# Kernel optimization log

Measured on AMD Instinct MI355X. Metric: run time of the kernel, lower is better.

The kernel has to match this reference:

```python
import jax, jax.numpy as jnp
import numpy as np

N_NODES = 50000
N_EDGES = 800000
EMB = 384            # EMBEDDING_DIM
NODE_F = EMB + 4     # 388
EDGE_F = EMB + 1     # 385
HEADS = 2
HID = 32             # per-head out_channels
HC = HEADS * HID     # 64
EDGE_IN = 2 * HC + EMB  # 512 classifier input
NEG_SLOPE = 0.2


def setup_inputs() -> dict:
    key = jax.random.key(0)
    ks = jax.random.split(key, 16)
    s = 0.05
    return {
        "x": jax.random.normal(ks[0], (N_NODES, NODE_F), dtype=jnp.float32),
        "edge_index": jax.random.randint(ks[1], (2, N_EDGES), 0, N_NODES, dtype=jnp.int32),
        "edge_attr": jax.random.uniform(ks[2], (N_EDGES, EDGE_F), dtype=jnp.float32),
        # GATv2Conv params
        "lin_l_w": jax.random.normal(ks[3], (NODE_F, HC), dtype=jnp.float32) * s,
        "lin_l_b": jnp.zeros((HC,), jnp.float32),
        "lin_r_w": jax.random.normal(ks[4], (NODE_F, HC), dtype=jnp.float32) * s,
        "lin_r_b": jnp.zeros((HC,), jnp.float32),
        "lin_e_w": jax.random.normal(ks[5], (EDGE_F, HC), dtype=jnp.float32) * s,
        "att": jax.random.normal(ks[6], (HEADS, HID), dtype=jnp.float32) * s,
        "conv_b": jnp.zeros((HC,), jnp.float32),
        # edge classifier MLP
        "mlp1_w": jax.random.normal(ks[7], (EDGE_IN, 64), dtype=jnp.float32) * s,
        "mlp1_b": jnp.zeros((64,), jnp.float32),
        "mlp2_w": jax.random.normal(ks[8], (64, 3), dtype=jnp.float32) * s,
        "mlp2_b": jnp.zeros((3,), jnp.float32),
    }


def _gatv2(x, edge_index, edge_attr, lin_l_w, lin_l_b, lin_r_w, lin_r_b,
           lin_e_w, att, conv_b):
    N = x.shape[0]
    src, tgt = edge_index[0], edge_index[1]
    # PyG add_self_loops with fill_value='mean': self-loop edge_attr is the
    # mean of incoming edge attributes per target node (0 if none).
    ones = jnp.ones((edge_attr.shape[0],), edge_attr.dtype)
    cnt = jax.ops.segment_sum(ones, tgt, num_segments=N)
    loop_attr = jax.ops.segment_sum(edge_attr, tgt, num_segments=N)
    loop_attr = loop_attr / jnp.maximum(cnt, 1.0)[:, None]
    ar = jnp.arange(N, dtype=src.dtype)
    src = jnp.concatenate([src, ar])
    tgt = jnp.concatenate([tgt, ar])
    ea = jnp.concatenate([edge_attr, loop_attr], axis=0)  # [E+N, EDGE_F]

    xl = (x @ lin_l_w + lin_l_b).reshape(N, HEADS, HID)  # source transform
    xr = (x @ lin_r_w + lin_r_b).reshape(N, HEADS, HID)  # target transform
    ee = (ea @ lin_e_w).reshape(-1, HEADS, HID)

    # GATv2 scoring: att . leaky_relu(x_j + x_i + e_ij)
    m = jax.nn.leaky_relu(xl[src] + xr[tgt] + ee, NEG_SLOPE)  # [E', H, C]
    score = jnp.einsum('ehc,hc->eh', m, att)                  # [E', H]
    # segment softmax over incoming edges of each target node
    smax = jax.ops.segment_max(score, tgt, num_segments=N)
    ex = jnp.exp(score - smax[tgt])
    ssum = jax.ops.segment_sum(ex, tgt, num_segments=N)
    alpha = ex / (ssum[tgt] + 1e-16)                          # [E', H]
    out = jax.ops.segment_sum(alpha[:, :, None] * xl[src], tgt, num_segments=N)
    return out.reshape(N, HC) + conv_b


def reference(x, edge_index, edge_attr, lin_l_w, lin_l_b, lin_r_w, lin_r_b,
              lin_e_w, att, conv_b, mlp1_w, mlp1_b, mlp2_w, mlp2_b):
    h = jax.nn.relu(_gatv2(x, edge_index, edge_attr, lin_l_w, lin_l_b,
                           lin_r_w, lin_r_b, lin_e_w, att, conv_b))
    # prediction edges == graph edges; query emb = edge_attr[:, :-1]
    src_e = h[edge_index[0]]
    tgt_e = h[edge_index[1]]
    q = edge_attr[:, :-1]
    e = jnp.concatenate([src_e, tgt_e, q], axis=1)  # [E, 512]
    e = jax.nn.relu(e @ mlp1_w + mlp1_b)
    logits = e @ mlp2_w + mlp2_b                    # [E, 3]
    probs = jax.nn.softmax(logits, axis=1)
    trust = 0.0 * probs[:, 0] + 0.5 * probs[:, 1] + 1.0 * probs[:, 2]
    return trust
```

## Files before the change

### kernel.cpp

```cpp
#include <hip/hip_runtime.h>

#define N_NODES 50000
#define N_EDGES 800000
#define NODE_F  388
#define EDGE_F  385
#define HC      64
#define KRED    384
#define NKT     6
#define NB      196

#define O_XLB     0L
#define O_XRB     1600000L
#define O_HAB     3200000L
#define O_HBB     4800000L
#define O_EXE     6400000L
#define O_EESUM   8000000L
#define O_SSUM    11200000L
#define O_DEG     11300000L
#define O_CURSOR  11350000L
#define O_ROWPTR  11410000L
#define O_BSUM    11470000L
#define O_CSRE    11480000L
#define O_CSRS    12280000L
#define O_CSRT    13080000L
#define O_WT      13900000L
#define O_WT2     13930000L
#define O_QW      13960000L

typedef __attribute__((ext_vector_type(8))) short bf8;
typedef __attribute__((ext_vector_type(4))) float f4;

typedef __attribute__((address_space(1))) const unsigned char ga_u8;
typedef __attribute__((address_space(3))) unsigned char lds_u8;

static __device__ __forceinline__ void gload_lds16(const void* g, void* l) {
    __builtin_amdgcn_global_load_lds((ga_u8*)g, (lds_u8*)l, 16, 0, 0);
}

static __device__ __forceinline__ unsigned short f2bf(float f) {
    unsigned u = __float_as_uint(f);
    u += 0x7FFFu + ((u >> 16) & 1u);
    return (unsigned short)(u >> 16);
}
static __device__ __forceinline__ float bf2f(unsigned short h) {
    return __uint_as_float(((unsigned)h) << 16);
}
static __device__ __forceinline__ unsigned cvtpk(float lo, float hi) {
    unsigned r;
    asm("v_cvt_pk_bf16_f32 %0, %1, %2" : "=v"(r) : "v"(lo), "v"(hi));
    return r;
}
static __device__ __forceinline__ void raw_barrier() {
    __builtin_amdgcn_sched_barrier(0);
    __builtin_amdgcn_s_barrier();
    __builtin_amdgcn_sched_barrier(0);
}

__global__ __launch_bounds__(256) void k_prep(
    const float* __restrict__ we, const float* __restrict__ w1,
    const float* __restrict__ wl, const float* __restrict__ wr,
    unsigned short* __restrict__ wt, unsigned short* __restrict__ wt2)
{
    int half = blockIdx.x / 96;
    int gid = (blockIdx.x - half * 96) * 256 + threadIdx.x;
    int c  = gid / 192;
    int k  = 2 * (gid - c * 192);
    float f0, f1;
    if (half == 0) {
        if (c < HC) {
            f0 = we[(long)k * HC + c];
            f1 = we[(long)(k + 1) * HC + c];
        } else {
            f0 = w1[(long)(128 + k) * HC + (c - HC)];
            f1 = w1[(long)(128 + k + 1) * HC + (c - HC)];
        }
        *(unsigned*)(wt + (long)c * KRED + k) =
            (unsigned)f2bf(f0) | ((unsigned)f2bf(f1) << 16);
    } else {
        const float* w = (c < HC) ? wl : wr;
        int cc = (c < HC) ? c : c - HC;
        f0 = w[(long)k * HC + cc];
        f1 = w[(long)(k + 1) * HC + cc];
        *(unsigned*)(wt2 + (long)c * KRED + k) =
            (unsigned)f2bf(f0) | ((unsigned)f2bf(f1) << 16);
    }
}

__global__ __launch_bounds__(256, 5) void k_node_lin(
    const float* __restrict__ x, const unsigned short* __restrict__ wt2,
    const float* __restrict__ wl, const float* __restrict__ wr,
    const float* __restrict__ bl, const float* __restrict__ br,
    unsigned short* __restrict__ xlb, unsigned short* __restrict__ xrb)
{
    __shared__ __align__(16) char W_s[2][16384];
    const int t = threadIdx.x;
    const int l = t & 63;
    const int w = t >> 6;
    const int n0 = blockIdx.x * 64;
    const int rb = (w & 1) * 32;
    const int cb = (w >> 1) * 64;
    const int lr = l & 15;
    const int lk = l >> 4;

    int wsrc[4];
#pragma unroll
    for (int i = 0; i < 4; ++i) {
        int c = w * 32 + i * 8 + (l >> 3);
        wsrc[i] = c * (KRED * 2) + ((((l & 7) * 16)) ^ ((l >> 3) << 4));
    }
    const char* wtb = (const char*)wt2;

    long rowx[2];
#pragma unroll
    for (int rg = 0; rg < 2; ++rg) {
        int n = n0 + rb + rg * 16 + lr;
        if (n >= N_NODES) n = N_NODES - 1;
        rowx[rg] = (long)n * NODE_F;
    }

    float af[2][16];
    bf8 fa[2][2];
    f4 acc[2][4];
#pragma unroll
    for (int rg = 0; rg < 2; ++rg)
#pragma unroll
        for (int cg = 0; cg < 4; ++cg) acc[rg][cg] = (f4)(0.f);

#define STAGE_W(kt, buf)                                                         \
    {                                                                            \
        _Pragma("unroll")                                                        \
        for (int i = 0; i < 4; ++i)                                              \
            gload_lds16(wtb + wsrc[i] + (kt) * 128, &W_s[buf][w * 4096 + i * 1024]); \
    }
#define ISSUE_AX(kt)                                                             \
    {                                                                            \
        _Pragma("unroll")                                                        \
        for (int rg = 0; rg < 2; ++rg) {                                         \
            const float* rp = x + rowx[rg] + (kt) * 64 + lk * 8;                 \
            float4 a0 = *(const float4*)(rp);                                    \
            float4 a1 = *(const float4*)(rp + 4);                                \
            float4 a2 = *(const float4*)(rp + 32);                               \
            float4 a3 = *(const float4*)(rp + 36);                               \
            af[rg][0]=a0.x; af[rg][1]=a0.y; af[rg][2]=a0.z; af[rg][3]=a0.w;      \
            af[rg][4]=a1.x; af[rg][5]=a1.y; af[rg][6]=a1.z; af[rg][7]=a1.w;      \
            af[rg][8]=a2.x; af[rg][9]=a2.y; af[rg][10]=a2.z; af[rg][11]=a2.w;    \
            af[rg][12]=a3.x; af[rg][13]=a3.y; af[rg][14]=a3.z; af[rg][15]=a3.w;  \
        }                                                                        \
    }
#define CVT_A()                                                                  \
    {                                                                            \
        _Pragma("unroll")                                                        \
        for (int rg = 0; rg < 2; ++rg)                                           \
            _Pragma("unroll")                                                    \
            for (int ks = 0; ks < 2; ++ks) {                                     \
                union { bf8 v; unsigned u[4]; } tu;                              \
                _Pragma("unroll")                                                \
                for (int p = 0; p < 4; ++p)                                      \
                    tu.u[p] = cvtpk(af[rg][ks * 8 + 2 * p], af[rg][ks * 8 + 2 * p + 1]); \
                fa[rg][ks] = tu.v;                                               \
            }                                                                    \
    }

    STAGE_W(0, 0);
    ISSUE_AX(0);

    for (int kt = 0; kt < NKT; ++kt) {
        const int buf = kt & 1;
        CVT_A();
        if (kt < NKT - 1) { STAGE_W(kt + 1, buf ^ 1); ISSUE_AX(kt + 1); }
        raw_barrier();
        __builtin_amdgcn_s_setprio(1);
#pragma unroll
        for (int ks = 0; ks < 2; ++ks) {
            const int kb = ks * 64 + lk * 16;
#pragma unroll
            for (int cg = 0; cg < 4; ++cg) {
                const int c = cb + cg * 16 + lr;
                bf8 b = *(bf8*)(&W_s[buf][c * 128 + (kb ^ ((c & 7) << 4))]);
                acc[0][cg] = __builtin_amdgcn_mfma_f32_16x16x32_bf16(fa[0][ks], b, acc[0][cg], 0, 0, 0);
                acc[1][cg] = __builtin_amdgcn_mfma_f32_16x16x32_bf16(fa[1][ks], b, acc[1][cg], 0, 0, 0);
            }
        }
        __builtin_amdgcn_s_setprio(0);
        raw_barrier();
    }

    const float* wsf = (cb == 0) ? wl : wr;
    const float* bsf = (cb == 0) ? bl : br;
    unsigned short* dst = (cb == 0) ? xlb : xrb;
    float wtail[4][4], bias[4];
#pragma unroll
    for (int cg = 0; cg < 4; ++cg) {
        int c = cg * 16 + lr;
        bias[cg] = bsf[c];
#pragma unroll
        for (int j = 0; j < 4; ++j)
            wtail[j][cg] = wsf[(long)(KRED + j) * HC + c];
    }
#pragma unroll
    for (int rg = 0; rg < 2; ++rg)
#pragma unroll
    for (int r = 0; r < 4; ++r) {
        const int n = n0 + rb + rg * 16 + lk * 4 + r;
        const int nc = (n < N_NODES) ? n : N_NODES - 1;
        float4 xt = *(const float4*)(x + (long)nc * NODE_F + KRED);
#pragma unroll
        for (int cg = 0; cg < 4; ++cg) {
            float v = acc[rg][cg][r] + bias[cg]
                    + xt.x * wtail[0][cg] + xt.y * wtail[1][cg]
                    + xt.z * wtail[2][cg] + xt.w * wtail[3][cg];
            float nb = __shfl_xor(v, 1);
            if (!(lr & 1) && n < N_NODES)
                *(unsigned*)&dst[(long)n * HC + cg * 16 + lr] = cvtpk(v, nb);
        }
    }
#undef STAGE_W
#undef ISSUE_AX
#undef CVT_A
}

__global__ __launch_bounds__(256) void k_hist(const int* __restrict__ ei, int* __restrict__ deg)
{
    int e = blockIdx.x * 256 + threadIdx.x;
    if (e < N_EDGES) atomicAdd(&deg[ei[N_EDGES + e]], 1);
}

__global__ __launch_bounds__(256) void k_scan_bsum(const int* __restrict__ deg, int* __restrict__ bsum)
{
    __shared__ int red[4];
    int i = blockIdx.x * 256 + threadIdx.x;
    int v = (i < N_NODES) ? deg[i] : 0;
    for (int m = 1; m < 64; m <<= 1) v += __shfl_xor(v, m);
    if ((threadIdx.x & 63) == 0) red[threadIdx.x >> 6] = v;
    __syncthreads();
    if (threadIdx.x == 0) bsum[blockIdx.x] = red[0] + red[1] + red[2] + red[3];
}

__global__ __launch_bounds__(256) void k_scan_boff(int* bsum)
{
    __shared__ int sc[256];
    int t = threadIdx.x;
    int v = (t < NB) ? bsum[t] : 0;
    sc[t] = v; __syncthreads();
    for (int off = 1; off < 256; off <<= 1) {
        int tv = (t >= off) ? sc[t - off] : 0;
        __syncthreads();
        sc[t] += tv;
        __syncthreads();
    }
    if (t < NB) bsum[t] = sc[t] - v;
}

__global__ __launch_bounds__(256) void k_scan_row(const int* __restrict__ deg,
                                                  const int* __restrict__ bsum,
                                                  int* __restrict__ rowptr)
{
    __shared__ int sc[256];
    int t = threadIdx.x;
    int i = blockIdx.x * 256 + t;
    int v = (i < N_NODES) ? deg[i] : 0;
    sc[t] = v; __syncthreads();
    for (int off = 1; off < 256; off <<= 1) {
        int tv = (t >= off) ? sc[t - off] : 0;
        __syncthreads();
        sc[t] += tv;
        __syncthreads();
    }
    if (i < N_NODES) rowptr[i] = bsum[blockIdx.x] + sc[t] - v;
    if (i == N_NODES - 1) rowptr[N_NODES] = N_EDGES;
}

__global__ __launch_bounds__(256) void k_scatter(const int* __restrict__ ei,
                                                 const int* __restrict__ rowptr,
                                                 int* __restrict__ cursor,
                                                 int* __restrict__ csr_e, int* __restrict__ csr_s,
                                                 int* __restrict__ csr_t)
{
    int e = blockIdx.x * 256 + threadIdx.x;
    if (e >= N_EDGES) return;
    int g = ei[N_EDGES + e];
    int pos = rowptr[g] + atomicAdd(&cursor[g], 1);
    csr_e[pos] = e;
    csr_s[pos] = ei[e];
    csr_t[pos] = g;
}

__global__ __launch_bounds__(256, 5) void k_edge_main(
    const float* __restrict__ ea,
    const int* __restrict__ csr_e, const int* __restrict__ csr_s, const int* __restrict__ csr_t,
    const unsigned short* __restrict__ wt, const float* __restrict__ we,
    const unsigned short* __restrict__ xlb, const unsigned short* __restrict__ xrb,
    const float* __restrict__ att,
    float* __restrict__ eesum, float* __restrict__ ssum,
    float* __restrict__ exPE, unsigned short* __restrict__ qWP)
{
    __shared__ __align__(16) char lds[32768];
    const int t = threadIdx.x;
    const int l = t & 63;
    const int w = t >> 6;
    const long pb = (long)blockIdx.x * 64;
    const int rb = (w & 1) * 32;
    const int cb = (w >> 1) * 64;
    const int lr = l & 15;
    const int lk = l >> 4;

    int wsrc[4];
#pragma unroll
    for (int i = 0; i < 4; ++i) {
        int c = w * 32 + i * 8 + (l >> 3);
        wsrc[i] = c * (KRED * 2) + ((((l & 7) * 16)) ^ ((l >> 3) << 4));
    }
    const char* wtb = (const char*)wt;

    unsigned rowb[2];
#pragma unroll
    for (int rg = 0; rg < 2; ++rg) {
        int e = csr_e[pb + rb + rg * 16 + lr];
        rowb[rg] = (unsigned)e * EDGE_F;
    }

    float af[2][16];
    bf8 fa[2][2];
    f4 acc[2][4];
#pragma unroll
    for (int rg = 0; rg < 2; ++rg)
#pragma unroll
        for (int cg = 0; cg < 4; ++cg) acc[rg][cg] = (f4)(0.f);

#define STAGE_W(kt, buf)                                                         \
    {                                                                            \
        _Pragma("unroll")                                                        \
        for (int i = 0; i < 4; ++i)                                              \
            gload_lds16(wtb + wsrc[i] + (kt) * 128,                              \
                        &lds[(buf) * 16384 + w * 4096 + i * 1024]);              \
    }

#define ISSUE_A(kt)                                                              \
    {                                                                            \
        _Pragma("unroll")                                                        \
        for (int rg = 0; rg < 2; ++rg) {                                         \
            const float* rp = ea + rowb[rg] + (kt) * 64 + lk * 8;                \
            _Pragma("unroll")                                                    \
            for (int q4 = 0; q4 < 4; ++q4)                                       \
                __builtin_memcpy(&af[rg][q4 * 4],                                \
                                 rp + (q4 >> 1) * 32 + (q4 & 1) * 4, 16);        \
        }                                                                        \
    }

#define CVT_A()                                                                  \
    {                                                                            \
        _Pragma("unroll")                                                        \
        for (int rg = 0; rg < 2; ++rg)                                           \
            _Pragma("unroll")                                                    \
            for (int ks = 0; ks < 2; ++ks) {                                     \
                union { bf8 v; unsigned u[4]; } tu;                              \
                _Pragma("unroll")                                                \
                for (int p = 0; p < 4; ++p)                                      \
                    tu.u[p] = cvtpk(af[rg][ks * 8 + 2 * p], af[rg][ks * 8 + 2 * p + 1]); \
                fa[rg][ks] = tu.v;                                               \
            }                                                                    \
    }

    STAGE_W(0, 0);
    ISSUE_A(0);

    for (int kt = 0; kt < NKT; ++kt) {
        const int buf = kt & 1;
        CVT_A();
        if (kt < NKT - 1) { STAGE_W(kt + 1, buf ^ 1); ISSUE_A(kt + 1); }
        raw_barrier();
        __builtin_amdgcn_s_setprio(1);
#pragma unroll
        for (int ks = 0; ks < 2; ++ks) {
            const int kb = ks * 64 + lk * 16;
#pragma unroll
            for (int cg = 0; cg < 4; ++cg) {
                const int c = cb + cg * 16 + lr;
                bf8 b = *(bf8*)(&lds[buf * 16384 + c * 128 + (kb ^ ((c & 7) << 4))]);
                acc[0][cg] = __builtin_amdgcn_mfma_f32_16x16x32_bf16(fa[0][ks], b, acc[0][cg], 0, 0, 0);
                acc[1][cg] = __builtin_amdgcn_mfma_f32_16x16x32_bf16(fa[1][ks], b, acc[1][cg], 0, 0, 0);
            }
        }
        __builtin_amdgcn_s_setprio(0);
        raw_barrier();
    }

    float (*ee_s)[65] = (float(*)[65])lds;
    int*   tgt_s      = (int*)(lds + 16640);
    float (*ex_s)[2]  = (float(*)[2])(lds + 16896);

    if (cb == 0) {
        float attv[4], w384[4];
#pragma unroll
        for (int cg = 0; cg < 4; ++cg) {
            attv[cg] = att[cg * 16 + lr];
            w384[cg] = we[(long)(EDGE_F - 1) * HC + cg * 16 + lr];
        }
#pragma unroll
        for (int rg = 0; rg < 2; ++rg)
#pragma unroll
        for (int r = 0; r < 4; ++r) {
            const int row = rb + rg * 16 + lk * 4 + r;
            const long p = pb + row;
            const int s = csr_s[p];
            const int g = csr_t[p];
            const float a384 = ea[(long)csr_e[p] * EDGE_F + (EDGE_F - 1)];
            float sc0 = 0.f, sc1 = 0.f;
#pragma unroll
            for (int cg = 0; cg < 4; ++cg) {
                const int c = cg * 16 + lr;
                float eev = fmaf(a384, w384[cg], acc[rg][cg][r]);
                ee_s[row][c] = eev;
                float m = eev + bf2f(xlb[(long)s * HC + c]) + bf2f(xrb[(long)g * HC + c]);
                float lv = m > 0.f ? m : 0.2f * m;
                float tm = lv * attv[cg];
                if (cg < 2) sc0 += tm; else sc1 += tm;
            }
            sc0 += __shfl_xor(sc0, 1); sc0 += __shfl_xor(sc0, 2);
            sc0 += __shfl_xor(sc0, 4); sc0 += __shfl_xor(sc0, 8);
            sc1 += __shfl_xor(sc1, 1); sc1 += __shfl_xor(sc1, 2);
            sc1 += __shfl_xor(sc1, 4); sc1 += __shfl_xor(sc1, 8);
            if (lr == 0) {
                float ex = __expf(sc0);
                exPE[p * 2 + 0] = ex;
                ex_s[row][0] = ex;
                tgt_s[row] = g;
            } else if (lr == 1) {
                float ex = __expf(sc1);
                exPE[p * 2 + 1] = ex;
                ex_s[row][1] = ex;
            }
        }
    } else {
#pragma unroll
        for (int rg = 0; rg < 2; ++rg)
#pragma unroll
        for (int r = 0; r < 4; ++r) {
            const long p = pb + rb + rg * 16 + lk * 4 + r;
#pragma unroll
            for (int cg = 0; cg < 4; ++cg) {
                float v = acc[rg][cg][r];
                float nb = __shfl_xor(v, 1);
                if (!(lr & 1)) {
                    unsigned pk = cvtpk(v, nb);
                    *(unsigned*)&qWP[p * HC + cg * 16 + lr] = pk;
                }
            }
        }
    }
    __syncthreads();

    {
        const int c = t & 63;
        const int q = t >> 6;
        const int r0 = q * 16;
        int   cur = tgt_s[r0];
        float run = ee_s[r0][c];
        for (int r = r0 + 1; r < r0 + 16; ++r) {
            int tg = tgt_s[r];
            if (tg != cur) {
                atomicAdd(&eesum[(long)cur * HC + c], run);
                run = 0.f; cur = tg;
            }
            run += ee_s[r][c];
        }
        atomicAdd(&eesum[(long)cur * HC + c], run);
        if (c < 2) {
            int   cur2 = tgt_s[r0];
            float run2 = ex_s[r0][c];
            for (int r = r0 + 1; r < r0 + 16; ++r) {
                int tg = tgt_s[r];
                if (tg != cur2) {
                    atomicAdd(&ssum[(long)cur2 * 2 + c], run2);
                    run2 = 0.f; cur2 = tg;
                }
                run2 += ex_s[r][c];
            }
            atomicAdd(&ssum[(long)cur2 * 2 + c], run2);
        }
    }
#undef STAGE_W
#undef ISSUE_A
#undef CVT_A
}

__global__ __launch_bounds__(256) void k_node_agg(
    const int* __restrict__ rowptr, const int* __restrict__ csr_s,
    const float* __restrict__ eesum, const float* __restrict__ ssum,
    const float* __restrict__ exPE,
    const unsigned short* __restrict__ xlb, const unsigned short* __restrict__ xrb,
    const float* __restrict__ att, const float* __restrict__ convb,
    const float* __restrict__ w1,
    unsigned short* __restrict__ hAb, unsigned short* __restrict__ hBb)
{
    const int lane = threadIdx.x & 63;
    const int n = blockIdx.x * 4 + (threadIdx.x >> 6);
    if (n >= N_NODES) return;
    const int p0 = rowptr[n], p1 = rowptr[n + 1];
    const int h = lane >> 5;
    const int deg = p1 - p0;

    float eeS = eesum[(long)n * HC + lane] / (deg > 0 ? (float)deg : 1.f);
    float sex = ssum[(long)n * 2 + h];

    float xlv = bf2f(xlb[(long)n * HC + lane]);
    float v = xlv + bf2f(xrb[(long)n * HC + lane]) + eeS;
    float lv = v > 0.f ? v : 0.2f * v;
    float partial = lv * att[lane];
    partial += __shfl_xor(partial, 1);
    partial += __shfl_xor(partial, 2);
    partial += __shfl_xor(partial, 4);
    partial += __shfl_xor(partial, 8);
    partial += __shfl_xor(partial, 16);
    float exSelf = __expf(partial);
    float inv = 1.f / (sex + exSelf + 1e-16f);
    float aggr = exSelf * inv * xlv;

#pragma unroll 2
    for (int p = p0; p < p1; ++p) {
        int s = csr_s[p];
        float alpha = exPE[(long)p * 2 + h] * inv;
        aggr = fmaf(alpha, bf2f(xlb[(long)s * HC + lane]), aggr);
    }

    float hv = fmaxf(aggr + convb[lane], 0.f);
    float accA = 0.f, accB = 0.f;
    for (int k = 0; k < 64; ++k) {
        float hb = __shfl(hv, k);
        accA = fmaf(hb, w1[k * HC + lane], accA);
        accB = fmaf(hb, w1[(64 + k) * HC + lane], accB);
    }
    hAb[(long)n * HC + lane] = f2bf(accA);
    hBb[(long)n * HC + lane] = f2bf(accB);
}

__global__ __launch_bounds__(256) void k_trust(
    const int* __restrict__ csr_e, const int* __restrict__ csr_s, const int* __restrict__ csr_t,
    const unsigned short* __restrict__ hAb, const unsigned short* __restrict__ hBb,
    const unsigned short* __restrict__ qWP, const float* __restrict__ b1,
    const float* __restrict__ w2, const float* __restrict__ b2,
    float* __restrict__ out)
{
    const long p = (long)blockIdx.x * 256 + threadIdx.x;
    const int s = csr_s[p];
    const int g = csr_t[p];
    const uint4* ha = (const uint4*)(hAb + (long)s * HC);
    const uint4* hb = (const uint4*)(hBb + (long)g * HC);
    const uint4* qw = (const uint4*)(qWP + p * HC);
    float a0 = 0.f, a1 = 0.f, a2 = 0.f;
#pragma unroll
    for (int ch = 0; ch < 8; ++ch) {
        uint4 ua = ha[ch], ub = hb[ch], uq = qw[ch];
        const unsigned* pa = (const unsigned*)&ua;
        const unsigned* pbb = (const unsigned*)&ub;
        const unsigned* pq = (const unsigned*)&uq;
#pragma unroll
        for (int j = 0; j < 4; ++j) {
            const int c = ch * 8 + j * 2;
            unsigned va = pa[j], vb = pbb[j], vq = pq[j];
            float m0 = __uint_as_float(va << 16) + __uint_as_float(vb << 16)
                     + __uint_as_float(vq << 16) + b1[c];
            float m1 = __uint_as_float(va & 0xffff0000u) + __uint_as_float(vb & 0xffff0000u)
                     + __uint_as_float(vq & 0xffff0000u) + b1[c + 1];
            m0 = fmaxf(m0, 0.f);
            m1 = fmaxf(m1, 0.f);
            a0 = fmaf(m0, w2[c * 3 + 0], a0); a0 = fmaf(m1, w2[c * 3 + 3], a0);
            a1 = fmaf(m0, w2[c * 3 + 1], a1); a1 = fmaf(m1, w2[c * 3 + 4], a1);
            a2 = fmaf(m0, w2[c * 3 + 2], a2); a2 = fmaf(m1, w2[c * 3 + 5], a2);
        }
    }
    float l0 = a0 + b2[0], l1 = a1 + b2[1], l2 = a2 + b2[2];
    float mx = fmaxf(l0, fmaxf(l1, l2));
    float e0 = __expf(l0 - mx), e1 = __expf(l1 - mx), e2 = __expf(l2 - mx);
    out[csr_e[p]] = (0.5f * e1 + e2) / (e0 + e1 + e2);
}

extern "C" void kernel_launch(void* const* d_in, const int* in_sizes, int n_in,
                              void* d_out, int out_size, void* d_ws, size_t ws_size,
                              hipStream_t stream)
{
    (void)in_sizes; (void)n_in; (void)out_size; (void)ws_size;
    const float* x     = (const float*)d_in[0];
    const int*   ei    = (const int*)  d_in[1];
    const float* ea    = (const float*)d_in[2];
    const float* wl    = (const float*)d_in[3];
    const float* bl    = (const float*)d_in[4];
    const float* wr    = (const float*)d_in[5];
    const float* br    = (const float*)d_in[6];
    const float* we    = (const float*)d_in[7];
    const float* att   = (const float*)d_in[8];
    const float* convb = (const float*)d_in[9];
    const float* w1    = (const float*)d_in[10];
    const float* b1    = (const float*)d_in[11];
    const float* w2    = (const float*)d_in[12];
    const float* b2    = (const float*)d_in[13];

    float* ws = (float*)d_ws;
    unsigned short* xlb = (unsigned short*)(ws + O_XLB);
    unsigned short* xrb = (unsigned short*)(ws + O_XRB);
    unsigned short* hAb = (unsigned short*)(ws + O_HAB);
    unsigned short* hBb = (unsigned short*)(ws + O_HBB);
    float* exPE   = ws + O_EXE;
    float* eesum  = ws + O_EESUM;
    float* ssum   = ws + O_SSUM;
    unsigned short* wt  = (unsigned short*)(ws + O_WT);
    unsigned short* wt2 = (unsigned short*)(ws + O_WT2);
    int* deg    = (int*)(ws + O_DEG);
    int* cursor = (int*)(ws + O_CURSOR);
    int* rowptr = (int*)(ws + O_ROWPTR);
    int* bsum   = (int*)(ws + O_BSUM);
    int* csr_e  = (int*)(ws + O_CSRE);
    int* csr_s  = (int*)(ws + O_CSRS);
    int* csr_t  = (int*)(ws + O_CSRT);
    unsigned short* qWP = (unsigned short*)(ws + O_QW);
    float* out  = (float*)d_out;

    hipMemsetAsync(ws + O_EESUM, 0, (size_t)(11400000L - O_EESUM) * sizeof(float), stream);

    k_prep<<<192, 256, 0, stream>>>(we, w1, wl, wr, wt, wt2);
    k_hist<<<3125, 256, 0, stream>>>(ei, deg);
    k_scan_bsum<<<NB, 256, 0, stream>>>(deg, bsum);
    k_scan_boff<<<1, 256, 0, stream>>>(bsum);
    k_scan_row<<<NB, 256, 0, stream>>>(deg, bsum, rowptr);
    k_scatter<<<3125, 256, 0, stream>>>(ei, rowptr, cursor, csr_e, csr_s, csr_t);
    k_node_lin<<<782, 256, 0, stream>>>(x, wt2, wl, wr, bl, br, xlb, xrb);
    k_edge_main<<<N_EDGES / 64, 256, 0, stream>>>(ea, csr_e, csr_s, csr_t, wt, we,
                                                  xlb, xrb, att, eesum, ssum, exPE, qWP);
    k_node_agg<<<N_NODES / 4, 256, 0, stream>>>(rowptr, csr_s, eesum, ssum, exPE,
                                                xlb, xrb, att, convb, w1, hAb, hBb);
    k_trust<<<3125, 256, 0, stream>>>(csr_e, csr_s, csr_t, hAb, hBb, qWP,
                                      b1, w2, b2, out);
}
```

Before: 884.3 us.

## Fuse weighted source aggregation into edge kernel and deepen A/W prefetch

The edge kernel now multiplies each edge's unnormalized exp score by the gathered source features and reduces them per target with run-length atomics into a new wsum buffer. The node aggregation kernel then only rescales by the softmax denominator, so the per-edge exPE array and the second CSR gather loop go away. Separately, the edge GEMM loop now prefetches two k-tiles ahead with double-buffered A registers, and the occupancy hint drops from 5 to 4 to make room for the extra registers. In exchange it adds 64 floats of atomic traffic per edge run, extra barriers in the edge kernel, and a larger memset.

```diff
diff --git a/kernel.cpp b/kernel.cpp
--- a/kernel.cpp
+++ b/kernel.cpp
@@ -13,19 +13,19 @@
 #define O_XRB     1600000L
 #define O_HAB     3200000L
 #define O_HBB     4800000L
-#define O_EXE     6400000L
-#define O_EESUM   8000000L
-#define O_SSUM    11200000L
-#define O_DEG     11300000L
-#define O_CURSOR  11350000L
-#define O_ROWPTR  11410000L
-#define O_BSUM    11470000L
-#define O_CSRE    11480000L
-#define O_CSRS    12280000L
-#define O_CSRT    13080000L
-#define O_WT      13900000L
-#define O_WT2     13930000L
-#define O_QW      13960000L
+#define O_EESUM   6400000L
+#define O_SSUM    9600000L
+#define O_WSUM    9700000L
+#define O_DEG     12900000L
+#define O_CURSOR  12950000L
+#define O_ROWPTR  13010000L
+#define O_BSUM    13070000L
+#define O_CSRE    13080000L
+#define O_CSRS    13880000L
+#define O_CSRT    14680000L
+#define O_WT      15500000L
+#define O_WT2     15530000L
+#define O_QW      15560000L
 
 typedef __attribute__((ext_vector_type(8))) short bf8;
 typedef __attribute__((ext_vector_type(4))) float f4;
@@ -147,7 +147,7 @@
             af[rg][12]=a3.x; af[rg][13]=a3.y; af[rg][14]=a3.z; af[rg][15]=a3.w;  \
         }                                                                        \
     }
-#define CVT_A()                                                                  \
+#define CVT_AX()                                                                 \
     {                                                                            \
         _Pragma("unroll")                                                        \
         for (int rg = 0; rg < 2; ++rg)                                           \
@@ -166,7 +166,7 @@
 
     for (int kt = 0; kt < NKT; ++kt) {
         const int buf = kt & 1;
-        CVT_A();
+        CVT_AX();
         if (kt < NKT - 1) { STAGE_W(kt + 1, buf ^ 1); ISSUE_AX(kt + 1); }
         raw_barrier();
         __builtin_amdgcn_s_setprio(1);
@@ -216,7 +216,7 @@
     }
 #undef STAGE_W
 #undef ISSUE_AX
-#undef CVT_A
+#undef CVT_AX
 }
 
 __global__ __launch_bounds__(256) void k_hist(const int* __restrict__ ei, int* __restrict__ deg)
@@ -285,14 +285,14 @@
     csr_t[pos] = g;
 }
 
-__global__ __launch_bounds__(256, 5) void k_edge_main(
+__global__ __launch_bounds__(256, 4) void k_edge_main(
     const float* __restrict__ ea,
     const int* __restrict__ csr_e, const int* __restrict__ csr_s, const int* __restrict__ csr_t,
     const unsigned short* __restrict__ wt, const float* __restrict__ we,
     const unsigned short* __restrict__ xlb, const unsigned short* __restrict__ xrb,
     const float* __restrict__ att,
-    float* __restrict__ eesum, float* __restrict__ ssum,
-    float* __restrict__ exPE, unsigned short* __restrict__ qWP)
+    float* __restrict__ eesum, float* __restrict__ ssum, float* __restrict__ wsum,
+    unsigned short* __restrict__ qWP)
 {
     __shared__ __align__(16) char lds[32768];
     const int t = threadIdx.x;
@@ -319,7 +319,7 @@
         rowb[rg] = (unsigned)e * EDGE_F;
     }
 
-    float af[2][16];
+    float af[2][2][16];
     bf8 fa[2][2];
     f4 acc[2][4];
 #pragma unroll
@@ -335,19 +335,19 @@
                         &lds[(buf) * 16384 + w * 4096 + i * 1024]);              \
     }
 
-#define ISSUE_A(kt)                                                              \
+#define ISSUE_A(b, kt)                                                           \
     {                                                                            \
         _Pragma("unroll")                                                        \
         for (int rg = 0; rg < 2; ++rg) {                                         \
             const float* rp = ea + rowb[rg] + (kt) * 64 + lk * 8;                \
             _Pragma("unroll")                                                    \
             for (int q4 = 0; q4 < 4; ++q4)                                       \
-                __builtin_memcpy(&af[rg][q4 * 4],                                \
+                __builtin_memcpy(&af[b][rg][q4 * 4],                             \
                                  rp + (q4 >> 1) * 32 + (q4 & 1) * 4, 16);        \
         }                                                                        \
     }
 
-#define CVT_A()                                                                  \
+#define CVT_A(b)                                                                 \
     {                                                                            \
         _Pragma("unroll")                                                        \
         for (int rg = 0; rg < 2; ++rg)                                           \
@@ -356,18 +356,18 @@
                 union { bf8 v; unsigned u[4]; } tu;                              \
                 _Pragma("unroll")                                                \
                 for (int p = 0; p < 4; ++p)                                      \
-                    tu.u[p] = cvtpk(af[rg][ks * 8 + 2 * p], af[rg][ks * 8 + 2 * p + 1]); \
+                    tu.u[p] = cvtpk(af[b][rg][ks * 8 + 2 * p],                   \
+                                    af[b][rg][ks * 8 + 2 * p + 1]);              \
                 fa[rg][ks] = tu.v;                                               \
             }                                                                    \
     }
 
-    STAGE_W(0, 0);
-    ISSUE_A(0);
+    STAGE_W(0, 0); ISSUE_A(0, 0);
+    STAGE_W(1, 1); ISSUE_A(1, 1);
 
     for (int kt = 0; kt < NKT; ++kt) {
-        const int buf = kt & 1;
-        CVT_A();
-        if (kt < NKT - 1) { STAGE_W(kt + 1, buf ^ 1); ISSUE_A(kt + 1); }
+        const int sl = kt & 1;
+        CVT_A(sl);
         raw_barrier();
         __builtin_amdgcn_s_setprio(1);
 #pragma unroll
@@ -376,13 +376,17 @@
 #pragma unroll
             for (int cg = 0; cg < 4; ++cg) {
                 const int c = cb + cg * 16 + lr;
-                bf8 b = *(bf8*)(&lds[buf * 16384 + c * 128 + (kb ^ ((c & 7) << 4))]);
+                bf8 b = *(bf8*)(&lds[sl * 16384 + c * 128 + (kb ^ ((c & 7) << 4))]);
                 acc[0][cg] = __builtin_amdgcn_mfma_f32_16x16x32_bf16(fa[0][ks], b, acc[0][cg], 0, 0, 0);
                 acc[1][cg] = __builtin_amdgcn_mfma_f32_16x16x32_bf16(fa[1][ks], b, acc[1][cg], 0, 0, 0);
             }
         }
         __builtin_amdgcn_s_setprio(0);
         raw_barrier();
+        if (kt + 2 < NKT) {
+            STAGE_W(kt + 2, sl);
+            ISSUE_A(sl, kt + 2);
+        }
     }
 
     float (*ee_s)[65] = (float(*)[65])lds;
@@ -421,14 +425,10 @@
             sc1 += __shfl_xor(sc1, 1); sc1 += __shfl_xor(sc1, 2);
             sc1 += __shfl_xor(sc1, 4); sc1 += __shfl_xor(sc1, 8);
             if (lr == 0) {
-                float ex = __expf(sc0);
-                exPE[p * 2 + 0] = ex;
-                ex_s[row][0] = ex;
+                ex_s[row][0] = __expf(sc0);
                 tgt_s[row] = g;
             } else if (lr == 1) {
-                float ex = __expf(sc1);
-                exPE[p * 2 + 1] = ex;
-                ex_s[row][1] = ex;
+                ex_s[row][1] = __expf(sc1);
             }
         }
     } else {
@@ -479,15 +479,53 @@
             atomicAdd(&ssum[(long)cur2 * 2 + c], run2);
         }
     }
+    __syncthreads();
+
+    if (cb == 0) {
+#pragma unroll
+        for (int rg = 0; rg < 2; ++rg)
+#pragma unroll
+        for (int r = 0; r < 4; ++r) {
+            const int row = rb + rg * 16 + lk * 4 + r;
+            const long p = pb + row;
+            const int s = csr_s[p];
+            const float ex0 = ex_s[row][0];
+            const float ex1 = ex_s[row][1];
+#pragma unroll
+            for (int cg = 0; cg < 4; ++cg) {
+                const int c = cg * 16 + lr;
+                float xv = bf2f(xlb[(long)s * HC + c]);
+                ee_s[row][c] = (cg < 2 ? ex0 : ex1) * xv;
+            }
+        }
+    }
+    __syncthreads();
+
+    {
+        const int c = t & 63;
+        const int q = t >> 6;
+        const int r0 = q * 16;
+        int   cur = tgt_s[r0];
+        float run = ee_s[r0][c];
+        for (int r = r0 + 1; r < r0 + 16; ++r) {
+            int tg = tgt_s[r];
+            if (tg != cur) {
+                atomicAdd(&wsum[(long)cur * HC + c], run);
+                run = 0.f; cur = tg;
+            }
+            run += ee_s[r][c];
+        }
+        atomicAdd(&wsum[(long)cur * HC + c], run);
+    }
 #undef STAGE_W
 #undef ISSUE_A
 #undef CVT_A
 }
 
 __global__ __launch_bounds__(256) void k_node_agg(
-    const int* __restrict__ rowptr, const int* __restrict__ csr_s,
+    const int* __restrict__ rowptr,
     const float* __restrict__ eesum, const float* __restrict__ ssum,
-    const float* __restrict__ exPE,
+    const float* __restrict__ wsum,
     const unsigned short* __restrict__ xlb, const unsigned short* __restrict__ xrb,
     const float* __restrict__ att, const float* __restrict__ convb,
     const float* __restrict__ w1,
@@ -496,9 +534,8 @@
     const int lane = threadIdx.x & 63;
     const int n = blockIdx.x * 4 + (threadIdx.x >> 6);
     if (n >= N_NODES) return;
-    const int p0 = rowptr[n], p1 = rowptr[n + 1];
     const int h = lane >> 5;
-    const int deg = p1 - p0;
+    const int deg = rowptr[n + 1] - rowptr[n];
 
     float eeS = eesum[(long)n * HC + lane] / (deg > 0 ? (float)deg : 1.f);
     float sex = ssum[(long)n * 2 + h];
@@ -514,14 +551,7 @@
     partial += __shfl_xor(partial, 16);
     float exSelf = __expf(partial);
     float inv = 1.f / (sex + exSelf + 1e-16f);
-    float aggr = exSelf * inv * xlv;
-
-#pragma unroll 2
-    for (int p = p0; p < p1; ++p) {
-        int s = csr_s[p];
-        float alpha = exPE[(long)p * 2 + h] * inv;
-        aggr = fmaf(alpha, bf2f(xlb[(long)s * HC + lane]), aggr);
-    }
+    float aggr = (exSelf * xlv + wsum[(long)n * HC + lane]) * inv;
 
     float hv = fmaxf(aggr + convb[lane], 0.f);
     float accA = 0.f, accB = 0.f;
@@ -600,9 +630,9 @@
     unsigned short* xrb = (unsigned short*)(ws + O_XRB);
     unsigned short* hAb = (unsigned short*)(ws + O_HAB);
     unsigned short* hBb = (unsigned short*)(ws + O_HBB);
-    float* exPE   = ws + O_EXE;
     float* eesum  = ws + O_EESUM;
     float* ssum   = ws + O_SSUM;
+    float* wsum   = ws + O_WSUM;
     unsigned short* wt  = (unsigned short*)(ws + O_WT);
     unsigned short* wt2 = (unsigned short*)(ws + O_WT2);
     int* deg    = (int*)(ws + O_DEG);
@@ -615,7 +645,7 @@
     unsigned short* qWP = (unsigned short*)(ws + O_QW);
     float* out  = (float*)d_out;
 
-    hipMemsetAsync(ws + O_EESUM, 0, (size_t)(11400000L - O_EESUM) * sizeof(float), stream);
+    hipMemsetAsync(ws + O_EESUM, 0, (size_t)(13000000L - O_EESUM) * sizeof(float), stream);
 
     k_prep<<<192, 256, 0, stream>>>(we, w1, wl, wr, wt, wt2);
     k_hist<<<3125, 256, 0, stream>>>(ei, deg);
@@ -625,8 +655,8 @@
     k_scatter<<<3125, 256, 0, stream>>>(ei, rowptr, cursor, csr_e, csr_s, csr_t);
     k_node_lin<<<782, 256, 0, stream>>>(x, wt2, wl, wr, bl, br, xlb, xrb);
     k_edge_main<<<N_EDGES / 64, 256, 0, stream>>>(ea, csr_e, csr_s, csr_t, wt, we,
-                                                  xlb, xrb, att, eesum, ssum, exPE, qWP);
-    k_node_agg<<<N_NODES / 4, 256, 0, stream>>>(rowptr, csr_s, eesum, ssum, exPE,
+                                                  xlb, xrb, att, eesum, ssum, wsum, qWP);
+    k_node_agg<<<N_NODES / 4, 256, 0, stream>>>(rowptr, eesum, ssum, wsum,
                                                 xlb, xrb, att, convb, w1, hAb, hBb);
     k_trust<<<3125, 256, 0, stream>>>(csr_e, csr_s, csr_t, hAb, hBb, qWP,
                                       b1, w2, b2, out);
```

New measurement: 749.5 us. 1.18x faster.
